# Performance work log

Hardware: AMD Instinct MI355X
Metric: run time of the kernel (lower is better)

The kernel has to match this reference:

```python
import jax, jax.numpy as jnp
import numpy as np

EPS = 1e-5

def _ln(z, g, b):
    # LayerNorm over last axis (per the gammas/betas of shape (2, 3H))
    mu = jnp.mean(z, axis=-1, keepdims=True)
    var = jnp.var(z, axis=-1, keepdims=True)
    return g * (z - mu) * jax.lax.rsqrt(var + EPS) + b

def setup_inputs() -> dict:
    key = jax.random.key(0)
    ks = jax.random.split(key, 12)
    B, L, D_IN, H, A, DEPTH = 64, 512, 256, 256, 128, 4
    glorot = lambda k, sh: jax.random.normal(k, sh, jnp.float32) * np.sqrt(2.0 / (sh[0] + sh[1])).astype(np.float32)
    # variable-length prefix masks (bucketing/masking semantics of the layer)
    lengths = jax.random.randint(ks[0], (B, 1), L // 2, L + 1)
    mask = jnp.arange(L)[None, :] < lengths
    return {
        'x': jax.random.normal(ks[1], (B, L, D_IN), jnp.float32),
        'mask': mask,
        'W_emb': glorot(ks[2], (D_IN, H)),
        'b_emb': jnp.zeros((H,), jnp.float32),
        'W': glorot(ks[3], (H, 3 * H)),
        'U': glorot(ks[4], (H, 3 * H)),
        'b': jnp.zeros((3 * H,), jnp.float32),
        'W_action_1': glorot(ks[5], (H, A)),
        'U_action_1': glorot(ks[6], (H, A)),
        'b_action_1': jnp.zeros((A,), jnp.float32),
        'W_action_2': glorot(ks[7], (A, 2)),
        'b_action_2': jnp.zeros((2,), jnp.float32),
        'gammas': jnp.ones((2, 3 * H), jnp.float32),
        'betas': jnp.zeros((2, 3 * H), jnp.float32),
        'depth': DEPTH,
    }

def _run_depth(x_seq, m_seq, W, U, b, Wa1, Ua1, ba1, Wa2, ba2, gammas, betas):
    # x_seq: (L,B,H), m_seq: (L,B) bool
    H = W.shape[0]
    B = x_seq.shape[1]
    # precompute + layernorm the input projection for all steps (fusable)
    xp_all = _ln(jnp.einsum('lbh,hk->lbk', x_seq, W), gammas[0], betas[0])  # (L,B,3H)

    def step(h, inputs):
        xp, xt, mt = inputs  # (B,3H), (B,H), (B,)
        hp = _ln(h @ U, gammas[1], betas[1])
        r = jax.nn.sigmoid(xp[:, :H] + hp[:, :H] + b[:H])
        z = jax.nn.sigmoid(xp[:, H:2 * H] + hp[:, H:2 * H] + b[H:2 * H])
        hh = jnp.tanh(xp[:, 2 * H:] + r * hp[:, 2 * H:] + b[2 * H:])
        h_new = z * h + (1.0 - z) * hh
        # action-policy subnetwork (binary merge/propagate decision)
        logits = jnp.tanh(xt @ Wa1 + h @ Ua1 + ba1) @ Wa2 + ba2  # (B,2)
        pol = jax.nn.softmax(logits, axis=-1)
        act = (pol[:, 1] > pol[:, 0]) & mt
        h_out = jnp.where(mt[:, None], h_new, h)  # masked steps carry state
        return h_out, (h_out, act, pol)

    h0 = jnp.zeros((B, H), x_seq.dtype)
    _, (h_seq, act_seq, pol_seq) = jax.lax.scan(step, h0, (xp_all, x_seq, m_seq))
    return h_seq, act_seq, pol_seq

def reference(x, mask, W_emb, b_emb, W, U, b, W_action_1, U_action_1, b_action_1,
              W_action_2, b_action_2, gammas, betas, depth):
    # embedding projection, then time-major like the Theano scans
    h_seq = jnp.swapaxes(x @ W_emb + b_emb, 0, 1)  # (L,B,H)
    m_seq = jnp.swapaxes(mask, 0, 1)               # (L,B)
    actions, policies = [], []
    for _ in range(depth):  # vertical (tree-depth) scan: small fixed count
        h_new, act, pol = _run_depth(h_seq, m_seq, W, U, b,
                                     W_action_1, U_action_1, b_action_1,
                                     W_action_2, b_action_2, gammas, betas)
        actions.append(act)
        policies.append(pol)
        h_seq = h_new
        m_seq = m_seq & act  # tree collapse: only selected nodes survive upward
    output = h_seq[-1]  # (B,H) final hidden state of top layer
    action = jnp.stack(actions, 0).transpose(2, 0, 1)      # (B,depth,L)
    policy = jnp.stack(policies, 0).transpose(2, 0, 1, 3)  # (B,depth,L,2)
    return output, action, policy
```

## Files before the change

kernel.cpp:

```cpp
#include <hip/hip_runtime.h>
#include <hip/hip_bf16.h>
#include <math.h>

#define BB 64
#define LL 512
#define HH 256
#define H3 768
#define AA 128
#define NDEPTH 4
#define NROWS (LL*BB)

#define EXCH_U64_PER_CHAIN (2 * 3 * 256)
#define EXCH_TOTAL_U64 (64 * EXCH_U64_PER_CHAIN)

typedef float vf32x32 __attribute__((ext_vector_type(32)));

__global__ void maskcvt_kernel(const unsigned char* __restrict__ raw,
                               int* __restrict__ m)
{
    int i = blockIdx.x * blockDim.x + threadIdx.x;
    bool bytemode = (raw[1] == 1);
    int v;
    if (bytemode) v = raw[i] ? 1 : 0;
    else          v = (((const int*)raw)[i] != 0) ? 1 : 0;
    m[i] = v;
}

__global__ __launch_bounds__(512) void mkidx_kernel(
    const int* __restrict__ m,
    int* __restrict__ rowidx,
    int* __restrict__ nact)
{
    const int b    = blockIdx.x;
    const int tid  = threadIdx.x;
    const int lane = tid & 63;
    const int w    = tid >> 6;
    __shared__ int wcnt[8];
    int pred = m[b * LL + tid];
    unsigned long long bal = __ballot(pred != 0);
    int below = __popcll(bal & ((1ull << lane) - 1ull));
    if (lane == 63) wcnt[w] = __popcll(bal);
    __syncthreads();
    int woff = 0;
#pragma unroll
    for (int i = 0; i < 8; ++i) woff += (i < w) ? wcnt[i] : 0;
    if (pred) rowidx[b * LL + woff + below] = tid;
    if (tid == 511) nact[b] = woff + wcnt[7];
}

template<int MODE, int EPI>
__global__ __launch_bounds__(256) void gemm_kernel(
    const float* __restrict__ A, const float* __restrict__ Bm,
    const float* __restrict__ bias,
    float* __restrict__ C, int M, int N,
    const int* __restrict__ ridx, const int* __restrict__ nact)
{
    __shared__ float As[16][136];
    __shared__ float Bs[16][136];
    const int tid = threadIdx.x;
    const int tx = tid & 15, ty = tid >> 4;
    const int row0 = blockIdx.y * 128, col0 = blockIdx.x * 128;

    int arow0 = 0, arow1 = 0;
    if (MODE == 3) {
        const int bb = row0 >> 9;
        const int na = nact[bb];
        if ((row0 & 511) >= na) return;
        const int r0 = row0 + (tid >> 2);
        const int r1 = r0 + 64;
        const int l0 = ((r0 & 511) < na) ? ridx[r0] : 0;
        const int l1 = ((r1 & 511) < na) ? ridx[r1] : 0;
        arow0 = l0 * 64 + bb;
        arow1 = l1 * 64 + bb;
    }

    float acc[8][8];
#pragma unroll
    for (int i = 0; i < 8; ++i)
#pragma unroll
        for (int j = 0; j < 8; ++j) acc[i][j] = 0.f;

    for (int kk = 0; kk < 256; kk += 16) {
#pragma unroll
        for (int i = 0; i < 2; ++i) {
            int aid = i * 256 + tid;
            int r   = aid >> 2;
            int k4  = (aid & 3) << 2;
            int rr  = row0 + r;
            float4 v;
            if (MODE == 1) {
                v = *(const float4*)(A + (rr & 63) * 131072 + (rr >> 6) * 256 + kk + k4);
            } else {
                int ar = i ? arow1 : arow0;
                v = *(const float4*)(A + ar * 256 + kk + k4);
            }
            As[k4 + 0][r] = v.x; As[k4 + 1][r] = v.y;
            As[k4 + 2][r] = v.z; As[k4 + 3][r] = v.w;

            int bid = i * 256 + tid;
            int bk  = bid >> 5;
            int c4  = (bid & 31) << 2;
            float4 w = *(const float4*)(Bm + (kk + bk) * N + col0 + c4);
            *(float4*)&Bs[bk][c4] = w;
        }
        __syncthreads();
#pragma unroll
        for (int k = 0; k < 16; ++k) {
            float a[8], bb2[8];
            *(float4*)&a[0]   = *(const float4*)&As[k][ty * 8];
            *(float4*)&a[4]   = *(const float4*)&As[k][ty * 8 + 4];
            *(float4*)&bb2[0] = *(const float4*)&Bs[k][tx * 8];
            *(float4*)&bb2[4] = *(const float4*)&Bs[k][tx * 8 + 4];
#pragma unroll
            for (int i = 0; i < 8; ++i)
#pragma unroll
                for (int j = 0; j < 8; ++j)
                    acc[i][j] += a[i] * bb2[j];
        }
        __syncthreads();
    }

#pragma unroll
    for (int i = 0; i < 8; ++i) {
        int row  = row0 + ty * 8 + i;
        int colb = col0 + tx * 8;
        float vout[8];
#pragma unroll
        for (int j = 0; j < 8; ++j) {
            float v = acc[i][j];
            if (EPI == 1) v += bias[colb + j];
            vout[j] = v;
        }
        *(float4*)&C[row * N + colb]     = *(float4*)&vout[0];
        *(float4*)&C[row * N + colb + 4] = *(float4*)&vout[4];
    }
}

__global__ __launch_bounds__(256) void lnrows_kernel(
    float* __restrict__ XP, const float* __restrict__ g0,
    const float* __restrict__ b0, const float* __restrict__ gb,
    const int* __restrict__ nact)
{
    const int row = blockIdx.x;
    if ((row & 511) >= nact[row >> 9]) return;
    const int tid = threadIdx.x;
    float* p = XP + (long)row * H3;
    float v0 = p[tid], v1 = p[tid + 256], v2 = p[tid + 512];
    float s = v0 + v1 + v2;
    float q = v0 * v0 + v1 * v1 + v2 * v2;
#pragma unroll
    for (int off = 32; off >= 1; off >>= 1) {
        s += __shfl_xor(s, off);
        q += __shfl_xor(q, off);
    }
    __shared__ float rs4[4], rq4[4];
    if ((tid & 63) == 0) { rs4[tid >> 6] = s; rq4[tid >> 6] = q; }
    __syncthreads();
    float S = rs4[0] + rs4[1] + rs4[2] + rs4[3];
    float Q = rq4[0] + rq4[1] + rq4[2] + rq4[3];
    float mu  = S * (1.f / 768.f);
    float var = Q * (1.f / 768.f) - mu * mu;
    float r   = rsqrtf(var + 1e-5f);
    p[tid]       = g0[tid]       * (v0 - mu) * r + b0[tid]       + gb[tid];
    p[tid + 256] = g0[tid + 256] * (v1 - mu) * r + b0[tid + 256] + gb[tid + 256];
    p[tid + 512] = g0[tid + 512] * (v2 - mu) * r + b0[tid + 512] + gb[tid + 512];
}

__global__ __launch_bounds__(512, 2) void scan3_kernel(
    const float* __restrict__ XP,
    const float* __restrict__ U,
    const float* __restrict__ g1, const float* __restrict__ b1,
    const int* __restrict__ mask,
    float* __restrict__ Y,
    unsigned long long* __restrict__ exch_f,
    unsigned long long* __restrict__ exch_s,
    int seq0,
    const float* __restrict__ Xc,
    const float* __restrict__ Wa1,
    const float* __restrict__ ba1,
    float* __restrict__ XA)
{
    __shared__ float h_cur[256];
    __shared__ float part[16][256];
    __shared__ float xp_lds[768];
    __shared__ float g1s[768], b1s[768];
    __shared__ int   mk[512];
    __shared__ float reds[4], redq[4];
    __shared__ float As[16][136];
    __shared__ float Bs[16][136];

    const int tid = threadIdx.x;

    if (blockIdx.x >= 192) {
        const int t    = blockIdx.x - 192;
        const int row0 = t * 128;
        const int tx   = tid & 15;
        const int ty4  = tid >> 4;
        float xacc[4][8];
#pragma unroll
        for (int i = 0; i < 4; ++i)
#pragma unroll
            for (int j = 0; j < 8; ++j) xacc[i][j] = 0.f;

        for (int kk = 0; kk < 256; kk += 16) {
            {
                int r  = tid >> 2;
                int k4 = (tid & 3) << 2;
                float4 v = *(const float4*)(Xc + (row0 + r) * 256 + kk + k4);
                As[k4 + 0][r] = v.x; As[k4 + 1][r] = v.y;
                As[k4 + 2][r] = v.z; As[k4 + 3][r] = v.w;
            }
            {
                int bk = tid >> 5;
                int c4 = (tid & 31) << 2;
                float4 w = *(const float4*)(Wa1 + (kk + bk) * AA + c4);
                *(float4*)&Bs[bk][c4] = w;
            }
            __syncthreads();
#pragma unroll
            for (int k = 0; k < 16; ++k) {
                float a[4], bb2[8];
                *(float4*)&a[0]   = *(const float4*)&As[k][ty4 * 4];
                *(float4*)&bb2[0] = *(const float4*)&Bs[k][tx * 8];
                *(float4*)&bb2[4] = *(const float4*)&Bs[k][tx * 8 + 4];
#pragma unroll
                for (int i = 0; i < 4; ++i)
#pragma unroll
                    for (int j = 0; j < 8; ++j)
                        xacc[i][j] += a[i] * bb2[j];
            }
            __syncthreads();
        }
#pragma unroll
        for (int i = 0; i < 4; ++i) {
            int row  = row0 + ty4 * 4 + i;
            int colb = tx * 8;
            float vout[8];
#pragma unroll
            for (int j = 0; j < 8; ++j) vout[j] = xacc[i][j] + ba1[colb + j];
            *(float4*)&XA[row * AA + colb]     = *(float4*)&vout[0];
            *(float4*)&XA[row * AA + colb + 4] = *(float4*)&vout[4];
        }
        return;
    }

    const int i0   = blockIdx.x;
    const int xcd  = i0 & 7;
    const int slot = i0 >> 3;
    const int b    = xcd + 8 * (slot / 3);
    const int s    = slot % 3;
    const int kg   = tid >> 5;
    const int cg   = tid & 31;
    const int q1   = (s + 1 >= 3) ? s - 2 : s + 1;
    const int q2   = (s + 2 >= 3) ? s - 1 : s + 2;

    vf32x32 u0v, u1v, u2v, u3v;
    {
        const volatile float* Uv = U;
        const int colbase = s * 256 + cg;
#pragma unroll
        for (int i = 0; i < 16; ++i) {
#pragma unroll
            for (int j = 0; j < 8; ++j) {
                const int f = i * 8 + j;
                float val = Uv[(kg * 16 + i) * H3 + colbase + 32 * j];
                if      (f < 32) u0v[f]      = val;
                else if (f < 64) u1v[f - 32] = val;
                else if (f < 96) u2v[f - 64] = val;
                else             u3v[f - 96] = val;
            }
        }
    }
    if (tid < 256) h_cur[tid] = 0.f;
    for (int i = tid; i < 768; i += 512) { g1s[i] = g1[i]; b1s[i] = b1[i]; }
    mk[tid] = mask[b * LL + tid];
    __syncthreads();

    unsigned long long* exbf = exch_f + b * EXCH_U64_PER_CHAIN;
    unsigned long long* exbs = exch_s + b * EXCH_U64_PER_CHAIN;
    int seq = seq0;
    int l2mode = (exch_f != exch_s) ? 1 : 0;

    for (int l = 0; l < LL; ++l) {
        if (!mk[l]) {
            if (s == 0 && tid < 64) {
                float4 hv = *(const float4*)&h_cur[tid * 4];
                *(float4*)&Y[((long)l * BB + b) * HH + tid * 4] = hv;
            }
            continue;
        }
        seq++;
        const int par = seq & 1;
        const int cs  = seq - seq0 - 1;

        float4 xr4;
        if (tid < 192) xr4 = *(const float4*)(XP + ((long)(b * LL + cs)) * H3 + tid * 4);

        float acc[8] = {0.f, 0.f, 0.f, 0.f, 0.f, 0.f, 0.f, 0.f};
#pragma unroll
        for (int i = 0; i < 4; ++i) {
            float4 hv = *(const float4*)&h_cur[kg * 16 + i * 4];
#pragma unroll
            for (int e = 0; e < 4; ++e) {
                const float hh = (e == 0) ? hv.x : (e == 1) ? hv.y
                               : (e == 2) ? hv.z : hv.w;
                const int ik = i * 4 + e;
#pragma unroll
                for (int j = 0; j < 8; ++j) {
                    const int f = ik * 8 + j;
                    const float uu = (f < 32) ? u0v[f]
                                   : (f < 64) ? u1v[f - 32]
                                   : (f < 96) ? u2v[f - 64]
                                   :            u3v[f - 96];
                    acc[j] += uu * hh;
                }
            }
        }
#pragma unroll
        for (int j = 0; j < 8; ++j)
            part[kg][cg + 32 * j] = acc[j];
        __syncthreads();

        if (tid < 192) *(float4*)&xp_lds[tid * 4] = xr4;

        float pre = 0.f, v0 = 0.f, v1 = 0.f, v2 = 0.f;
        if (tid < 256) {
            pre = part[0][tid];
#pragma unroll
            for (int gg = 1; gg < 16; ++gg) pre += part[gg][tid];

            unsigned long long pk =
                ((unsigned long long)(unsigned)seq << 32) |
                (unsigned long long)__float_as_uint(pre);
            const int eo = (par * 3 + s) * 256 + tid;
            const int e1 = (par * 3 + q1) * 256 + tid;
            const int e2 = (par * 3 + q2) * 256 + tid;
            asm volatile("global_store_dwordx2 %0, %1, off"
                         :: "v"((unsigned long long)(exbf + eo)), "v"(pk)
                         : "memory");
            __hip_atomic_store(exbs + eo, pk, __ATOMIC_RELAXED,
                               __HIP_MEMORY_SCOPE_AGENT);

            unsigned long long x1 = 0, x2 = 0;
            bool d1 = false, d2 = false;
            if (l2mode) {
                int spins = 0;
                while (spins < 48) {
                    unsigned long long t1, t2;
                    asm volatile("global_load_dwordx2 %0, %2, off sc0\n\t"
                                 "global_load_dwordx2 %1, %3, off sc0\n\t"
                                 "s_waitcnt vmcnt(0)"
                                 : "=&v"(t1), "=&v"(t2)
                                 : "v"((unsigned long long)(exbf + e1)),
                                   "v"((unsigned long long)(exbf + e2))
                                 : "memory");
                    if (!d1 && (int)(t1 >> 32) == seq) { x1 = t1; d1 = true; }
                    if (!d2 && (int)(t2 >> 32) == seq) { x2 = t2; d2 = true; }
                    if (d1 && d2) break;
                    ++spins;
                }
                if (!(d1 && d2)) l2mode = 0;
            }
            if (!(d1 && d2)) {
                int spins = 0;
                do {
                    unsigned long long t1 =
                        __hip_atomic_load(exbs + e1, __ATOMIC_RELAXED,
                                          __HIP_MEMORY_SCOPE_AGENT);
                    unsigned long long t2 =
                        __hip_atomic_load(exbs + e2, __ATOMIC_RELAXED,
                                          __HIP_MEMORY_SCOPE_AGENT);
                    if (!d1 && (int)(t1 >> 32) == seq) { x1 = t1; d1 = true; }
                    if (!d2 && (int)(t2 >> 32) == seq) { x2 = t2; d2 = true; }
                    if (++spins > 8) __builtin_amdgcn_s_sleep(1);
                } while (!(d1 && d2));
            }
            float w1 = __uint_as_float((unsigned)x1);
            float w2 = __uint_as_float((unsigned)x2);
            v0 = (s == 0) ? pre : ((q1 == 0) ? w1 : w2);
            v1 = (s == 1) ? pre : ((q1 == 1) ? w1 : w2);
            v2 = (s == 2) ? pre : ((q1 == 2) ? w1 : w2);

            float st = v0 + v1 + v2;
            float qt = v0 * v0 + v1 * v1 + v2 * v2;
#pragma unroll
            for (int off = 32; off >= 1; off >>= 1) {
                st += __shfl_xor(st, off);
                qt += __shfl_xor(qt, off);
            }
            if ((tid & 63) == 0) { reds[tid >> 6] = st; redq[tid >> 6] = qt; }
        }
        __syncthreads();

        if (tid < 256) {
            float S = reds[0] + reds[1] + reds[2] + reds[3];
            float Q = redq[0] + redq[1] + redq[2] + redq[3];
            float mu = S * (1.f / 768.f);
            float rs = rsqrtf(Q * (1.f / 768.f) - mu * mu + 1e-5f);
            float hp_r = g1s[tid]       * (v0 - mu) * rs + b1s[tid];
            float hp_z = g1s[256 + tid] * (v1 - mu) * rs + b1s[256 + tid];
            float hp_h = g1s[512 + tid] * (v2 - mu) * rs + b1s[512 + tid];
            float xr = xp_lds[tid], xz = xp_lds[256 + tid], xh = xp_lds[512 + tid];
            float r  = 1.f / (1.f + expf(-(xr + hp_r)));
            float z  = 1.f / (1.f + expf(-(xz + hp_z)));
            float hh = tanhf(xh + r * hp_h);
            float o  = z * h_cur[tid] + (1.f - z) * hh;
            h_cur[tid] = o;
            if (s == 0) Y[((long)l * BB + b) * HH + tid] = o;
        }
        __syncthreads();
    }
}

__global__ __launch_bounds__(256) void gemmact_kernel(
    const float* __restrict__ Yprev,
    const float* __restrict__ Ua1,
    const float* __restrict__ XA,
    const float* __restrict__ Wa2,
    const float* __restrict__ ba2,
    const int* __restrict__ mask_in, int* __restrict__ mask_out,
    float* __restrict__ act_out, float* __restrict__ pol_out, int d)
{
    __shared__ float As[16][136];
    __shared__ float Bs[16][136];
    const int tid = threadIdx.x;
    const int tx = tid & 15, ty = tid >> 4;
    const int row0 = blockIdx.y * 128;

    float acc[8][8];
#pragma unroll
    for (int i = 0; i < 8; ++i)
#pragma unroll
        for (int j = 0; j < 8; ++j) acc[i][j] = 0.f;

    for (int kk = 0; kk < 256; kk += 16) {
#pragma unroll
        for (int i = 0; i < 2; ++i) {
            int aid = i * 256 + tid;
            int r   = aid >> 2;
            int k4  = (aid & 3) << 2;
            int rr  = row0 + r;
            float4 v;
            if (rr < 64) v = make_float4(0.f, 0.f, 0.f, 0.f);
            else         v = *(const float4*)(Yprev + (rr - 64) * 256 + kk + k4);
            As[k4 + 0][r] = v.x; As[k4 + 1][r] = v.y;
            As[k4 + 2][r] = v.z; As[k4 + 3][r] = v.w;

            int bid = i * 256 + tid;
            int bk  = bid >> 5;
            int c4  = (bid & 31) << 2;
            float4 w = *(const float4*)(Ua1 + (kk + bk) * AA + c4);
            *(float4*)&Bs[bk][c4] = w;
        }
        __syncthreads();
#pragma unroll
        for (int k = 0; k < 16; ++k) {
            float a[8], bb2[8];
            *(float4*)&a[0]   = *(const float4*)&As[k][ty * 8];
            *(float4*)&a[4]   = *(const float4*)&As[k][ty * 8 + 4];
            *(float4*)&bb2[0] = *(const float4*)&Bs[k][tx * 8];
            *(float4*)&bb2[4] = *(const float4*)&Bs[k][tx * 8 + 4];
#pragma unroll
            for (int i = 0; i < 8; ++i)
#pragma unroll
                for (int j = 0; j < 8; ++j)
                    acc[i][j] += a[i] * bb2[j];
        }
        __syncthreads();
    }

    float p0[8], p1[8];
#pragma unroll
    for (int i = 0; i < 8; ++i) { p0[i] = 0.f; p1[i] = 0.f; }
#pragma unroll
    for (int i = 0; i < 8; ++i) {
        int row  = row0 + ty * 8 + i;
#pragma unroll
        for (int j = 0; j < 8; ++j) {
            int c   = tx * 8 + j;
            float v = tanhf(acc[i][j] + XA[row * AA + c]);
            p0[i] += v * Wa2[c * 2];
            p1[i] += v * Wa2[c * 2 + 1];
        }
    }
#pragma unroll
    for (int off = 1; off < 16; off <<= 1) {
#pragma unroll
        for (int i = 0; i < 8; ++i) {
            p0[i] += __shfl_xor(p0[i], off);
            p1[i] += __shfl_xor(p1[i], off);
        }
    }
    if (tx == 0) {
#pragma unroll
        for (int i = 0; i < 8; ++i) {
            int row = row0 + ty * 8 + i;
            int l   = row >> 6, bb = row & 63;
            float l0 = p0[i] + ba2[0];
            float l1 = p1[i] + ba2[1];
            float m  = fmaxf(l0, l1);
            float e0 = expf(l0 - m), e1 = expf(l1 - m);
            float inv = 1.f / (e0 + e1);
            float q0 = e0 * inv, q1v = e1 * inv;
            int mt = mask_in[bb * LL + l];
            int a  = (q1v > q0) && mt;
            act_out[bb * (NDEPTH * LL) + d * LL + l] = a ? 1.f : 0.f;
            pol_out[bb * (NDEPTH * LL * 2) + d * (LL * 2) + l * 2 + 0] = q0;
            pol_out[bb * (NDEPTH * LL * 2) + d * (LL * 2) + l * 2 + 1] = q1v;
            mask_out[bb * LL + l] = a;
        }
    }
}

__global__ void final_copy_kernel(const float* __restrict__ X, float* __restrict__ out)
{
    int i = blockIdx.x * blockDim.x + threadIdx.x;
    int bb = i >> 8, j = i & 255;
    out[i] = X[((long)(LL - 1) * BB + bb) * HH + j];
}

extern "C" void kernel_launch(void* const* d_in, const int* in_sizes, int n_in,
                              void* d_out, int out_size, void* d_ws, size_t ws_size,
                              hipStream_t stream)
{
    const float* x      = (const float*)d_in[0];
    const void*  mraw   = d_in[1];
    const float* W_emb  = (const float*)d_in[2];
    const float* b_emb  = (const float*)d_in[3];
    const float* W      = (const float*)d_in[4];
    const float* U      = (const float*)d_in[5];
    const float* bias3  = (const float*)d_in[6];
    const float* Wa1    = (const float*)d_in[7];
    const float* Ua1    = (const float*)d_in[8];
    const float* ba1    = (const float*)d_in[9];
    const float* Wa2    = (const float*)d_in[10];
    const float* ba2    = (const float*)d_in[11];
    const float* gammas = (const float*)d_in[12];
    const float* betas  = (const float*)d_in[13];

    float* out = (float*)d_out;
    char*  ws  = (char*)d_ws;

    float* XP = (float*)(ws);
    float* X  = (float*)(ws + 100663296UL);
    float* Y  = (float*)(ws + 134217728UL);
    float* XA = (float*)(ws + 167772160UL);
    int*   m0 = (int*)(ws + 184549376UL);
    int*   m1 = (int*)(ws + 184680448UL);
    unsigned long long* exch_f = (unsigned long long*)(ws + 184811520UL);
    unsigned long long* exch_s =
        (ws_size >= 184811520UL + 2UL * 786432UL)
            ? exch_f + EXCH_TOTAL_U64 : exch_f;

    float* act_out = out + BB * HH;
    float* pol_out = act_out + BB * NDEPTH * LL;

    maskcvt_kernel<<<dim3(NROWS / 256), dim3(256), 0, stream>>>(
        (const unsigned char*)mraw, m0);

    gemm_kernel<1, 1><<<dim3(2, 256), dim3(256), 0, stream>>>(
        x, W_emb, b_emb, X, NROWS, HH, nullptr, nullptr);

    float* Xc = X; float* Yc = Y;
    int* mc = m0; int* mn = m1;

    for (int d = 0; d < NDEPTH; ++d) {
        int* rowidx = (int*)Yc;
        int* nactp  = ((int*)Yc) + NROWS;

        mkidx_kernel<<<dim3(BB), dim3(512), 0, stream>>>(mc, rowidx, nactp);

        gemm_kernel<3, 0><<<dim3(6, 256), dim3(256), 0, stream>>>(
            Xc, W, nullptr, XP, NROWS, H3, rowidx, nactp);
        lnrows_kernel<<<dim3(NROWS), dim3(256), 0, stream>>>(
            XP, gammas, betas, bias3, nactp);

        scan3_kernel<<<dim3(448), dim3(512), 0, stream>>>(
            XP, U, gammas + H3, betas + H3, mc, Yc, exch_f, exch_s, d << 10,
            Xc, Wa1, ba1, XA);

        gemmact_kernel<<<dim3(1, 256), dim3(256), 0, stream>>>(
            Yc, Ua1, XA, Wa2, ba2, mc, mn, act_out, pol_out, d);

        { float* tmp = Xc; Xc = Yc; Yc = tmp; }
        { int* tmp = mc; mc = mn; mn = tmp; }
    }

    final_copy_kernel<<<dim3(BB), dim3(256), 0, stream>>>(Xc, out);
}
```

Before: 3.296 ms.

## Probe L2 exchange path at startup, prefetch next XP row, use lightweight barriers

Before the recurrence, each block writes a tagged hello value to the fast exchange buffer and polls its two peers' slots, enabling the L2 fast path only if the handshake succeeds. The spin budget rises on the first step. The XP row for the next step is now loaded after the exchange so its latency overlaps the spin wait instead of sitting on the critical path. __syncthreads is replaced by an lgkmcnt-only wait plus s_barrier, so outstanding global stores no longer stall the barrier, and exchange stores now use sc0. The risks are extra startup polling and depending on the weaker barrier being enough for correctness.

```diff
diff --git a/kernel.cpp b/kernel.cpp
--- a/kernel.cpp
+++ b/kernel.cpp
@@ -12,6 +12,8 @@
 
 #define EXCH_U64_PER_CHAIN (2 * 3 * 256)
 #define EXCH_TOTAL_U64 (64 * EXCH_U64_PER_CHAIN)
+
+#define BARRIER_LGKM() asm volatile("s_waitcnt lgkmcnt(0)\n\ts_barrier" ::: "memory")
 
 typedef float vf32x32 __attribute__((ext_vector_type(32)));
 
@@ -254,6 +256,18 @@
     const int q1   = (s + 1 >= 3) ? s - 2 : s + 1;
     const int q2   = (s + 2 >= 3) ? s - 1 : s + 2;
 
+    unsigned long long* exbf = exch_f + b * EXCH_U64_PER_CHAIN;
+    unsigned long long* exbs = exch_s + b * EXCH_U64_PER_CHAIN;
+    const int split = (exch_f != exch_s);
+    const unsigned long long hello =
+        ((unsigned long long)(unsigned)(seq0 + 600) << 32) | 0x48454C4Cull;
+
+    if (split && tid < 256) {
+        asm volatile("global_store_dwordx2 %0, %1, off sc0"
+                     :: "v"((unsigned long long)(exbf + s * 256 + tid)),
+                        "v"(hello) : "memory");
+    }
+
     vf32x32 u0v, u1v, u2v, u3v;
     {
         const volatile float* Uv = U;
@@ -274,12 +288,33 @@
     if (tid < 256) h_cur[tid] = 0.f;
     for (int i = tid; i < 768; i += 512) { g1s[i] = g1[i]; b1s[i] = b1[i]; }
     mk[tid] = mask[b * LL + tid];
-    __syncthreads();
-
-    unsigned long long* exbf = exch_f + b * EXCH_U64_PER_CHAIN;
-    unsigned long long* exbs = exch_s + b * EXCH_U64_PER_CHAIN;
+    BARRIER_LGKM();
+
+    int l2mode = 0;
+    if (split && tid < 256) {
+        const unsigned long long* f1 = exbf + q1 * 256 + tid;
+        const unsigned long long* f2 = exbf + q2 * 256 + tid;
+        int ok1 = 0, ok2 = 0;
+        for (int it = 0; it < 256 && !(ok1 & ok2); ++it) {
+            unsigned long long t1, t2;
+            asm volatile("global_load_dwordx2 %0, %2, off sc0\n\t"
+                         "global_load_dwordx2 %1, %3, off sc0\n\t"
+                         "s_waitcnt vmcnt(0)"
+                         : "=&v"(t1), "=&v"(t2)
+                         : "v"((unsigned long long)f1),
+                           "v"((unsigned long long)f2)
+                         : "memory");
+            ok1 |= (t1 == hello);
+            ok2 |= (t2 == hello);
+        }
+        l2mode = ok1 & ok2;
+    }
+
+    float4 xr4 = make_float4(0.f, 0.f, 0.f, 0.f);
+    if (tid < 192)
+        xr4 = *(const float4*)(XP + ((long)(b * LL)) * H3 + tid * 4);
+
     int seq = seq0;
-    int l2mode = (exch_f != exch_s) ? 1 : 0;
 
     for (int l = 0; l < LL; ++l) {
         if (!mk[l]) {
@@ -292,9 +327,6 @@
         seq++;
         const int par = seq & 1;
         const int cs  = seq - seq0 - 1;
-
-        float4 xr4;
-        if (tid < 192) xr4 = *(const float4*)(XP + ((long)(b * LL + cs)) * H3 + tid * 4);
 
         float acc[8] = {0.f, 0.f, 0.f, 0.f, 0.f, 0.f, 0.f, 0.f};
 #pragma unroll
@@ -319,7 +351,7 @@
 #pragma unroll
         for (int j = 0; j < 8; ++j)
             part[kg][cg + 32 * j] = acc[j];
-        __syncthreads();
+        BARRIER_LGKM();
 
         if (tid < 192) *(float4*)&xp_lds[tid * 4] = xr4;
 
@@ -335,7 +367,7 @@
             const int eo = (par * 3 + s) * 256 + tid;
             const int e1 = (par * 3 + q1) * 256 + tid;
             const int e2 = (par * 3 + q2) * 256 + tid;
-            asm volatile("global_store_dwordx2 %0, %1, off"
+            asm volatile("global_store_dwordx2 %0, %1, off sc0"
                          :: "v"((unsigned long long)(exbf + eo)), "v"(pk)
                          : "memory");
             __hip_atomic_store(exbs + eo, pk, __ATOMIC_RELAXED,
@@ -344,8 +376,9 @@
             unsigned long long x1 = 0, x2 = 0;
             bool d1 = false, d2 = false;
             if (l2mode) {
+                const int budget = (cs == 0) ? 2048 : 128;
                 int spins = 0;
-                while (spins < 48) {
+                while (spins < budget) {
                     unsigned long long t1, t2;
                     asm volatile("global_load_dwordx2 %0, %2, off sc0\n\t"
                                  "global_load_dwordx2 %1, %3, off sc0\n\t"
@@ -375,6 +408,12 @@
                     if (++spins > 8) __builtin_amdgcn_s_sleep(1);
                 } while (!(d1 && d2));
             }
+
+            if (tid < 192) {
+                int nr = cs + 1; if (nr > 511) nr = 511;
+                xr4 = *(const float4*)(XP + ((long)(b * LL + nr)) * H3 + tid * 4);
+            }
+
             float w1 = __uint_as_float((unsigned)x1);
             float w2 = __uint_as_float((unsigned)x2);
             v0 = (s == 0) ? pre : ((q1 == 0) ? w1 : w2);
@@ -390,7 +429,7 @@
             }
             if ((tid & 63) == 0) { reds[tid >> 6] = st; redq[tid >> 6] = qt; }
         }
-        __syncthreads();
+        BARRIER_LGKM();
 
         if (tid < 256) {
             float S = reds[0] + reds[1] + reds[2] + reds[3];
@@ -408,7 +447,7 @@
             h_cur[tid] = o;
             if (s == 0) Y[((long)l * BB + b) * HH + tid] = o;
         }
-        __syncthreads();
+        BARRIER_LGKM();
     }
 }
 
```

New measurement: 4.393 ms. +33.3%, slower.
